# Kernel tuning notes

Hardware: AMD Instinct MI355X
Metric: run time of the kernel (lower is better)

Reference implementation:

```python
import jax, jax.numpy as jnp
import numpy as np

HF = 14            # qubits (hidden_features)
SPECTRUM = 3       # spectrum_layer (data re-uploading blocks)
NSTEPS = 2         # N outer iterations
SEL_L = 3          # StronglyEntanglingLayers depth per block (weights1[..., 3, HF, 3])
DIM = 2 ** HF
BN_EPS = 1e-5

# wire 0 = most-significant bit (PennyLane default.qubit convention)
_bits = ((np.arange(DIM)[:, None] >> (HF - 1 - np.arange(HF))[None, :]) & 1)  # (DIM, HF)
Z_SIGNS = (1.0 - 2.0 * _bits).astype(np.float32)      # +1 for |0>, -1 for |1>
RZ_SIGNS = -Z_SIGNS                                    # (2b-1): RZ phase sign per wire
# CZ ring sign vectors for ranges r=1..SEL_L: (-1)^{sum_j b_j * b_{(j+r)%HF}}
_cz = []
for r in range(1, SEL_L + 1):
    parity = (_bits * _bits[:, (np.arange(HF) + r) % HF]).sum(axis=1) % 2
    _cz.append((1.0 - 2.0 * parity).astype(np.float32))
CZ_SIGNS = np.stack(_cz)  # (SEL_L, DIM)


def _rot_matrix(phi, theta, omega):
    # Rot = RZ(omega) @ RY(theta) @ RZ(phi)
    c = jnp.cos(theta / 2)
    s = jnp.sin(theta / 2)
    ep = jnp.exp(-0.5j * (phi + omega))
    em = jnp.exp(-0.5j * (phi - omega))
    return jnp.array([[ep * c, -jnp.conj(em) * s],
                      [em * s, jnp.conj(ep) * c]])


def _apply_1q(state, U, wire):
    # state: (b, 2^HF) complex; apply 2x2 U on `wire`
    b = state.shape[0]
    st = state.reshape(b, 2 ** wire, 2, -1)
    st = jnp.einsum('pq,bwqm->bwpm', U, st)
    return st.reshape(b, DIM)


def _run_circuit(x, w):
    # x: (b, HF) real RZ angles; w: (SPECTRUM, SEL_L, HF, 3)
    b = x.shape[0]
    state = jnp.zeros((b, DIM), jnp.complex64).at[:, 0].set(1.0)
    rz_diag = jnp.exp(0.5j * (x @ jnp.asarray(RZ_SIGNS).T))  # (b, DIM) complex64
    cz = jnp.asarray(CZ_SIGNS)
    for i in range(SPECTRUM):
        state = state * rz_diag                 # RZ(x_j) on every wire (diagonal)
        for l in range(SEL_L):
            for q in range(HF):
                state = _apply_1q(state, _rot_matrix(w[i, l, q, 0], w[i, l, q, 1], w[i, l, q, 2]), q)
            state = state * cz[l][None, :]      # CZ ring, range l+1 (diagonal +-1)
    probs = jnp.abs(state) ** 2
    return probs @ jnp.asarray(Z_SIGNS)          # <Z_j> per wire, (b, HF)


def setup_inputs() -> dict:
    key = jax.random.key(0)
    ks = jax.random.split(key, 6)
    b, c, w, h = 64, 1, 28, 28
    input_dim = c * w * h
    x = jax.random.normal(ks[0], (b, c, w, h), dtype=jnp.float32)
    w_down = jax.random.normal(ks[1], (HF, input_dim), dtype=jnp.float32) * (1.0 / np.sqrt(input_dim))
    b_down = jax.random.normal(ks[2], (HF,), dtype=jnp.float32) * 0.01
    bn_w = jnp.ones((HF,), jnp.float32)
    bn_b = jnp.zeros((HF,), jnp.float32)
    weights1 = jax.random.normal(ks[3], (NSTEPS, SPECTRUM, SEL_L, HF, 3), dtype=jnp.float32) * 0.4
    w_up = jax.random.normal(ks[4], (input_dim, HF), dtype=jnp.float32) * (1.0 / np.sqrt(HF))
    b_up = jax.random.normal(ks[5], (input_dim,), dtype=jnp.float32) * 0.01
    return {"x": x, "w_down": w_down, "b_down": b_down, "bn_w": bn_w, "bn_b": bn_b,
            "weights1": weights1, "w_up": w_up, "b_up": b_up}


def reference(x, w_down, b_down, bn_w, bn_b, weights1, w_up, b_up):
    b, c, w, h = x.shape
    xr = x.reshape(b, -1) @ w_down.T + b_down          # linear_down -> (b, HF)
    for n in range(NSTEPS):
        mu = xr.mean(axis=0)
        var = ((xr - mu) ** 2).mean(axis=0)            # BatchNorm1d, training-mode batch stats
        xr = (xr - mu) / jnp.sqrt(var + BN_EPS) * bn_w + bn_b
        xr = _run_circuit(xr, weights1[n])             # quantum circuit expvals -> (b, HF)
    out = xr @ w_up.T + b_up                           # linear_up
    return out.reshape(b, c, w, h)
```

## Files before the change

kernel.cpp:

```cpp
#include <hip/hip_runtime.h>
#include <math.h>

#define INV2PI 0.15915494309189535f

typedef _Float16 f16;
typedef _Float16 f16x8 __attribute__((ext_vector_type(8)));
typedef _Float16 f16x4 __attribute__((ext_vector_type(4)));
typedef float f32x16 __attribute__((ext_vector_type(16)));

#define Z16 {0.f,0.f,0.f,0.f,0.f,0.f,0.f,0.f,0.f,0.f,0.f,0.f,0.f,0.f,0.f,0.f}

#define WS_MATS 0
#define WS_TABS 262144
#define WS_RY1  266240
#define WS_XR   266304
#define WS_XR2  267200

__global__ void k_pre(const float* __restrict__ w1, float* __restrict__ ws)
{
    int blk = blockIdx.x, t = threadIdx.x;
    if (blk < 32) {
        int n = blk >> 4, rem = blk & 15, k = (rem >> 1) + 2, side = rem & 1;
        __shared__ float R[7][2][2];
        if (t < 7) {
            int wire = side ? (13 - t) : (6 - t);
            float th = w1[n*378 + (k-1)*42 + wire*3 + 1];
            float s, c; sincosf(0.5f*th, &s, &c);
            R[t][0][0] = c;  R[t][0][1] = -s;
            R[t][1][0] = s;  R[t][1][1] = c;
        }
        __syncthreads();
        f16* M = (f16*)ws + blk * 16384;
        for (int e = t; e < 16384; e += 256) {
            int tile = e >> 12, kk = (e >> 9) & 7, l = (e >> 3) & 63, j = e & 7;
            int row = tile*32 + (l & 31);
            int col = kk*16 + (l >> 5)*8 + j;
            float v = 1.f;
            #pragma unroll
            for (int bi = 0; bi < 7; ++bi) v *= R[bi][(row>>bi)&1][(col>>bi)&1];
            M[e] = (f16)v;
        }
    } else if (blk == 32) {
        for (int e = t; e < 4096; e += 256) {
            int n = e >> 11, r = e & 2047, k = (r >> 8) + 1;
            int r2 = r & 255, side = r2 >> 7, v = r2 & 127;
            float acc = 0.f;
            #pragma unroll
            for (int bi = 0; bi < 7; ++bi) {
                if ((v >> bi) & 1) {
                    int wire = side ? (13 - bi) : (6 - bi);
                    acc += (w1[n*378 + (k-1)*42 + wire*3 + 2]
                          + w1[n*378 + k*42     + wire*3 + 0]) * INV2PI;
                }
            }
            ws[WS_TABS + ((n*8 + (k-1))*2 + side)*128 + v] = acc;
        }
    } else {
        if (t < 28) {
            int n = t / 14, q = t % 14;
            float th = w1[n*378 + q*3 + 1];
            float s, c; sincosf(0.5f*th, &s, &c);
            ws[WS_RY1 + (n*14 + q)*2 + 0] = c;
            ws[WS_RY1 + (n*14 + q)*2 + 1] = s;
        }
    }
}

__global__ void k_down(const float* __restrict__ x, const float* __restrict__ wd,
                       const float* __restrict__ bd, float* __restrict__ xr)
{
    int row  = blockIdx.x;
    int wave = threadIdx.x >> 6;
    int lane = threadIdx.x & 63;
    const float* xrow = x + row * 784;
    for (int f = wave; f < 14; f += 4) {
        const float* wrow = wd + f * 784;
        float s = 0.f;
        for (int j = lane; j < 784; j += 64) s = fmaf(xrow[j], wrow[j], s);
        #pragma unroll
        for (int off = 32; off; off >>= 1) s += __shfl_xor(s, off);
        if (lane == 0) xr[row * 14 + f] = s + bd[f];
    }
}

template<int WHICH>
__global__ __launch_bounds__(1024, 4)
void k_circuit(const f16* __restrict__ matsg, const float* __restrict__ tabsg,
               const float* __restrict__ ry1g, const float* __restrict__ xrin,
               float* __restrict__ xrout, const float* __restrict__ bnw,
               const float* __restrict__ bnb, const float* __restrict__ wu,
               const float* __restrict__ bu)
{
    __shared__ __align__(16) ushort SRe[16384];
    __shared__ __align__(16) ushort SIm[16384];
    __shared__ __align__(16) ushort IRe[16384];
    __shared__ __align__(16) ushort IIm[16384];
    __shared__ float2 ETAB[8][2][128];
    __shared__ float PA[128], PB[128];
    __shared__ float XR[896];
    __shared__ float XROW[14];
    __shared__ float RED[16][15];

    const int row = blockIdx.x, T = threadIdx.x;
    const int w = T >> 6, l = T & 63, lm = l & 31, hb = l >> 5;
    const int tm = w >> 2, tn = w & 3;
    const int mrow = tm*32 + lm, nn = tn*32 + lm;

    for (int i = T; i < 896; i += 1024) XR[i] = xrin[i];
    __syncthreads();
    if (T < 14) {
        float mu = 0.f;
        for (int r = 0; r < 64; ++r) mu += XR[r*14 + T];
        mu *= (1.f/64.f);
        float var = 0.f;
        for (int r = 0; r < 64; ++r) { float d = XR[r*14 + T] - mu; var += d*d; }
        var *= (1.f/64.f);
        float xb = (XR[row*14 + T] - mu) * rsqrtf(var + 1e-5f) * bnw[T] + bnb[T];
        XROW[T] = xb * INV2PI;
    }
    __syncthreads();
    for (int e = T; e < 2048; e += 1024) {
        int k0 = e >> 8, r2 = e & 255, side = r2 >> 7, v = r2 & 127;
        float val = tabsg[(k0*2 + side)*128 + v];
        if (k0 == 2 || k0 == 5) {
            #pragma unroll
            for (int bi = 0; bi < 7; ++bi)
                if ((v >> bi) & 1) val += XROW[side ? (13-bi) : (6-bi)];
        }
        float fr = __builtin_amdgcn_fractf(val);
        ETAB[k0][side][v] = make_float2(__builtin_amdgcn_cosf(fr),
                                        __builtin_amdgcn_sinf(fr));
    }
    if (T < 256) {
        int side = T >> 7, v = T & 127;
        float p = 1.f;
        #pragma unroll
        for (int bi = 0; bi < 7; ++bi) {
            int wire = side ? (13-bi) : (6-bi);
            p *= ((v >> bi) & 1) ? ry1g[wire*2 + 1] : ry1g[wire*2];
        }
        if (side) PB[v] = p; else PA[v] = p;
    }
    __syncthreads();
    {
        int a = T >> 3, b0 = (T & 7) << 4;
        float2 eA = ETAB[0][0][a];
        float pav = PA[a];
        #pragma unroll
        for (int g = 0; g < 2; ++g) {
            f16 hr[8], hm[8];
            #pragma unroll
            for (int u = 0; u < 8; ++u) {
                int b = b0 + g*8 + u;
                int d = (a << 7) | b;
                int rot = ((d >> 1) | (d << 13)) & 16383;
                float2 eB = ETAB[0][1][b];
                float zr = eA.x*eB.x - eA.y*eB.y;
                float zi = eA.x*eB.y + eA.y*eB.x;
                if (__popc(d & rot) & 1) { zr = -zr; zi = -zi; }
                float mg = pav * PB[b];
                hr[u] = (f16)(mg * zr);
                hm[u] = (f16)(mg * zi);
            }
            int hoff = ((a << 7) + b0 + g*8) ^ ((a & 15) << 3);
            f16x8 vr = {hr[0],hr[1],hr[2],hr[3],hr[4],hr[5],hr[6],hr[7]};
            f16x8 vi = {hm[0],hm[1],hm[2],hm[3],hm[4],hm[5],hm[6],hm[7]};
            *(f16x8*)((f16*)SRe + hoff) = vr;
            *(f16x8*)((f16*)SIm + hoff) = vi;
        }
    }
    __syncthreads();

    #pragma unroll 1
    for (int k = 2; k <= 9; ++k) {
        const int P = k & 1;
        const f16* M1 = matsg + ((k-2)*2 + (P ? 0 : 1)) * 16384;
        const f16* M2 = matsg + ((k-2)*2 + (P ? 1 : 0)) * 16384;
        f32x16 ar = Z16, ai = Z16;
        #pragma unroll
        for (int kk = 0; kk < 8; ++kk) {
            f16x8 B = *(const f16x8*)(M1 + (tn*8 + kk)*512 + l*8);
            int c  = kk*16 + hb*8;
            int sa = ((mrow << 7) + c) ^ ((mrow & 15) << 3);
            f16x8 Ar = *(const f16x8*)((const f16*)SRe + sa);
            f16x8 Ai = *(const f16x8*)((const f16*)SIm + sa);
            ar = __builtin_amdgcn_mfma_f32_32x32x16_f16(Ar, B, ar, 0,0,0);
            ai = __builtin_amdgcn_mfma_f32_32x32x16_f16(Ai, B, ai, 0,0,0);
        }
        #pragma unroll
        for (int g = 0; g < 4; ++g) {
            int mb = tm*32 + g*8 + hb*4;
            int hoff = ((nn << 7) + mb) ^ ((nn & 15) << 3);
            f16x4 vr = {(f16)ar[g*4],(f16)ar[g*4+1],(f16)ar[g*4+2],(f16)ar[g*4+3]};
            f16x4 vi = {(f16)ai[g*4],(f16)ai[g*4+1],(f16)ai[g*4+2],(f16)ai[g*4+3]};
            *(f16x4*)((f16*)IRe + hoff) = vr;
            *(f16x4*)((f16*)IIm + hoff) = vi;
        }
        __syncthreads();
        f32x16 dr = Z16, di = Z16;
        #pragma unroll
        for (int kk = 0; kk < 8; ++kk) {
            f16x8 A = *(const f16x8*)(M2 + (tm*8 + kk)*512 + l*8);
            int c  = kk*16 + hb*8;
            int s0 = ((nn << 7) + c) ^ ((nn & 15) << 3);
            f16x8 Br = *(const f16x8*)((const f16*)IRe + s0);
            f16x8 Bi = *(const f16x8*)((const f16*)IIm + s0);
            dr = __builtin_amdgcn_mfma_f32_32x32x16_f16(A, Br, dr, 0,0,0);
            di = __builtin_amdgcn_mfma_f32_32x32x16_f16(A, Bi, di, 0,0,0);
        }
        if (k < 9) {
            float2 eN = ETAB[k-1][P ? 0 : 1][nn];
            const int czr = ((k-1) % 3) + 1;
            #pragma unroll
            for (int g = 0; g < 4; ++g) {
                float prf[4], pif[4];
                #pragma unroll
                for (int u = 0; u < 4; ++u) {
                    int r = g*4 + u;
                    int mloc = (r & 3) + 8*(r >> 2) + 4*hb;
                    int mg = tm*32 + mloc;
                    float2 eM = ETAB[k-1][P ? 1 : 0][mg];
                    int d = P ? ((nn << 7) | mg) : ((mg << 7) | nn);
                    int rot = ((d >> czr) | (d << (14 - czr))) & 16383;
                    float zr = eM.x*eN.x - eM.y*eN.y;
                    float zi = eM.x*eN.y + eM.y*eN.x;
                    if (__popc(d & rot) & 1) { zr = -zr; zi = -zi; }
                    float re = dr[r], im = di[r];
                    prf[u] = re*zr - im*zi;
                    pif[u] = re*zi + im*zr;
                }
                int mb = tm*32 + g*8 + hb*4;
                int hoff = ((nn << 7) + mb) ^ ((nn & 15) << 3);
                f16x4 vr = {(f16)prf[0],(f16)prf[1],(f16)prf[2],(f16)prf[3]};
                f16x4 vi = {(f16)pif[0],(f16)pif[1],(f16)pif[2],(f16)pif[3]};
                *(f16x4*)((f16*)SRe + hoff) = vr;
                *(f16x4*)((f16*)SIm + hoff) = vi;
            }
        } else {
            float tot = 0.f;
            float bs[14];
            #pragma unroll
            for (int i = 0; i < 14; ++i) bs[i] = 0.f;
            float tp = 0.f, s0 = 0.f, s1v = 0.f, s3 = 0.f, s4 = 0.f;
            #pragma unroll
            for (int r = 0; r < 16; ++r) {
                float re = dr[r], im = di[r];
                float p = fmaf(re, re, im*im);
                tp += p;
                if (r & 1) s0  += p;
                if (r & 2) s1v += p;
                if (r & 4) s3  += p;
                if (r & 8) s4  += p;
            }
            tot += tp;
            bs[0] += s0; bs[1] += s1v; bs[3] += s3; bs[4] += s4;
            if (hb)     bs[2] += tp;
            if (tm & 1) bs[5] += tp;
            if (tm & 2) bs[6] += tp;
            #pragma unroll
            for (int i = 0; i < 7; ++i)
                if ((nn >> i) & 1) bs[7+i] += tp;
            #pragma unroll
            for (int off = 32; off; off >>= 1) {
                tot += __shfl_xor(tot, off);
                #pragma unroll
                for (int i = 0; i < 14; ++i) bs[i] += __shfl_xor(bs[i], off);
            }
            if (l == 0) {
                #pragma unroll
                for (int i = 0; i < 14; ++i) RED[w][i] = bs[i];
                RED[w][14] = tot;
            }
        }
        __syncthreads();
    }

    if (T < 14) {
        float tt = 0.f, ss = 0.f;
        #pragma unroll
        for (int ww = 0; ww < 16; ++ww) { tt += RED[ww][14]; ss += RED[ww][13 - T]; }
        float val = tt - 2.f * ss;
        XROW[T] = val;
        if (WHICH == 0) xrout[row*14 + T] = val;
    }
    __syncthreads();
    if (WHICH == 1) {
        for (int j = T; j < 784; j += 1024) {
            float s = bu[j];
            #pragma unroll
            for (int f = 0; f < 14; ++f) s = fmaf(XROW[f], wu[j*14 + f], s);
            xrout[row*784 + j] = s;
        }
    }
}

extern "C" void kernel_launch(void* const* d_in, const int* in_sizes, int n_in,
                              void* d_out, int out_size, void* d_ws, size_t ws_size,
                              hipStream_t stream)
{
    const float* x  = (const float*)d_in[0];
    const float* wd = (const float*)d_in[1];
    const float* bd = (const float*)d_in[2];
    const float* bw = (const float*)d_in[3];
    const float* bb = (const float*)d_in[4];
    const float* w1 = (const float*)d_in[5];
    const float* wu = (const float*)d_in[6];
    const float* bu = (const float*)d_in[7];
    float* out = (float*)d_out;
    float* ws  = (float*)d_ws;

    hipLaunchKernelGGL(k_pre,  dim3(34), dim3(256), 0, stream, w1, ws);
    hipLaunchKernelGGL(k_down, dim3(64), dim3(256), 0, stream, x, wd, bd, ws + WS_XR);

    const f16* mats0 = (const f16*)ws;
    const f16* mats1 = (const f16*)ws + 262144;
    hipLaunchKernelGGL(k_circuit<0>, dim3(64), dim3(1024), 0, stream,
                       mats0, ws + WS_TABS, ws + WS_RY1,
                       ws + WS_XR, ws + WS_XR2, bw, bb, wu, bu);
    hipLaunchKernelGGL(k_circuit<1>, dim3(64), dim3(1024), 0, stream,
                       mats1, ws + WS_TABS + 2048, ws + WS_RY1 + 28,
                       ws + WS_XR2, out, bw, bb, wu, bu);
}
```

Before: 124.3 us.

## Halve circuit block size and give each wave a 32x64 MFMA tile

The circuit kernel drops from 1024 to 512 threads per block. Each wave now computes two 32x32 output tiles, so one LDS A-fragment load feeds two MFMA pairs, which cuts LDS read traffic per MFMA. s_setprio is raised around the MFMA loops to favour the matrix issue. The trade-offs are fewer waves to hide latency, higher register pressure from four accumulators, and more serial work per thread in the setup phases.

```diff
diff --git a/kernel.cpp b/kernel.cpp
--- a/kernel.cpp
+++ b/kernel.cpp
@@ -84,7 +84,7 @@
 }
 
 template<int WHICH>
-__global__ __launch_bounds__(1024, 4)
+__global__ __launch_bounds__(512, 2)
 void k_circuit(const f16* __restrict__ matsg, const float* __restrict__ tabsg,
                const float* __restrict__ ry1g, const float* __restrict__ xrin,
                float* __restrict__ xrout, const float* __restrict__ bnw,
@@ -99,14 +99,14 @@
     __shared__ float PA[128], PB[128];
     __shared__ float XR[896];
     __shared__ float XROW[14];
-    __shared__ float RED[16][15];
+    __shared__ float RED[8][15];
 
     const int row = blockIdx.x, T = threadIdx.x;
     const int w = T >> 6, l = T & 63, lm = l & 31, hb = l >> 5;
-    const int tm = w >> 2, tn = w & 3;
-    const int mrow = tm*32 + lm, nn = tn*32 + lm;
-
-    for (int i = T; i < 896; i += 1024) XR[i] = xrin[i];
+    const int th = w >> 1, tp = w & 1;
+    const int hrow = th*32 + lm;
+
+    for (int i = T; i < 896; i += 512) XR[i] = xrin[i];
     __syncthreads();
     if (T < 14) {
         float mu = 0.f;
@@ -119,7 +119,7 @@
         XROW[T] = xb * INV2PI;
     }
     __syncthreads();
-    for (int e = T; e < 2048; e += 1024) {
+    for (int e = T; e < 2048; e += 512) {
         int k0 = e >> 8, r2 = e & 255, side = r2 >> 7, v = r2 & 127;
         float val = tabsg[(k0*2 + side)*128 + v];
         if (k0 == 2 || k0 == 5) {
@@ -143,11 +143,11 @@
     }
     __syncthreads();
     {
-        int a = T >> 3, b0 = (T & 7) << 4;
+        int a = T >> 2, b0 = (T & 3) << 5;
         float2 eA = ETAB[0][0][a];
         float pav = PA[a];
         #pragma unroll
-        for (int g = 0; g < 2; ++g) {
+        for (int g = 0; g < 4; ++g) {
             f16 hr[8], hm[8];
             #pragma unroll
             for (int u = 0; u < 8; ++u) {
@@ -176,90 +176,117 @@
         const int P = k & 1;
         const f16* M1 = matsg + ((k-2)*2 + (P ? 0 : 1)) * 16384;
         const f16* M2 = matsg + ((k-2)*2 + (P ? 1 : 0)) * 16384;
-        f32x16 ar = Z16, ai = Z16;
+        f32x16 ar0 = Z16, ai0 = Z16, ar1 = Z16, ai1 = Z16;
+        __builtin_amdgcn_s_setprio(1);
         #pragma unroll
         for (int kk = 0; kk < 8; ++kk) {
-            f16x8 B = *(const f16x8*)(M1 + (tn*8 + kk)*512 + l*8);
+            f16x8 B0 = *(const f16x8*)(M1 + ((tp*2+0)<<12) + kk*512 + l*8);
+            f16x8 B1 = *(const f16x8*)(M1 + ((tp*2+1)<<12) + kk*512 + l*8);
             int c  = kk*16 + hb*8;
-            int sa = ((mrow << 7) + c) ^ ((mrow & 15) << 3);
+            int sa = ((hrow << 7) + c) ^ ((hrow & 15) << 3);
             f16x8 Ar = *(const f16x8*)((const f16*)SRe + sa);
             f16x8 Ai = *(const f16x8*)((const f16*)SIm + sa);
-            ar = __builtin_amdgcn_mfma_f32_32x32x16_f16(Ar, B, ar, 0,0,0);
-            ai = __builtin_amdgcn_mfma_f32_32x32x16_f16(Ai, B, ai, 0,0,0);
-        }
-        #pragma unroll
-        for (int g = 0; g < 4; ++g) {
-            int mb = tm*32 + g*8 + hb*4;
-            int hoff = ((nn << 7) + mb) ^ ((nn & 15) << 3);
-            f16x4 vr = {(f16)ar[g*4],(f16)ar[g*4+1],(f16)ar[g*4+2],(f16)ar[g*4+3]};
-            f16x4 vi = {(f16)ai[g*4],(f16)ai[g*4+1],(f16)ai[g*4+2],(f16)ai[g*4+3]};
-            *(f16x4*)((f16*)IRe + hoff) = vr;
-            *(f16x4*)((f16*)IIm + hoff) = vi;
+            ar0 = __builtin_amdgcn_mfma_f32_32x32x16_f16(Ar, B0, ar0, 0,0,0);
+            ai0 = __builtin_amdgcn_mfma_f32_32x32x16_f16(Ai, B0, ai0, 0,0,0);
+            ar1 = __builtin_amdgcn_mfma_f32_32x32x16_f16(Ar, B1, ar1, 0,0,0);
+            ai1 = __builtin_amdgcn_mfma_f32_32x32x16_f16(Ai, B1, ai1, 0,0,0);
+        }
+        __builtin_amdgcn_s_setprio(0);
+        #pragma unroll
+        for (int j = 0; j < 2; ++j) {
+            int nj = (tp*2 + j)*32 + lm;
+            const f32x16& vr = j ? ar1 : ar0;
+            const f32x16& vi = j ? ai1 : ai0;
+            #pragma unroll
+            for (int g = 0; g < 4; ++g) {
+                int mb = th*32 + g*8 + hb*4;
+                int hoff = ((nj << 7) + mb) ^ ((nj & 15) << 3);
+                f16x4 hr = {(f16)vr[g*4],(f16)vr[g*4+1],(f16)vr[g*4+2],(f16)vr[g*4+3]};
+                f16x4 hi = {(f16)vi[g*4],(f16)vi[g*4+1],(f16)vi[g*4+2],(f16)vi[g*4+3]};
+                *(f16x4*)((f16*)IRe + hoff) = hr;
+                *(f16x4*)((f16*)IIm + hoff) = hi;
+            }
         }
         __syncthreads();
-        f32x16 dr = Z16, di = Z16;
+        f32x16 dr0 = Z16, di0 = Z16, dr1 = Z16, di1 = Z16;
+        __builtin_amdgcn_s_setprio(1);
         #pragma unroll
         for (int kk = 0; kk < 8; ++kk) {
-            f16x8 A = *(const f16x8*)(M2 + (tm*8 + kk)*512 + l*8);
+            f16x8 A0 = *(const f16x8*)(M2 + ((tp*2+0)<<12) + kk*512 + l*8);
+            f16x8 A1 = *(const f16x8*)(M2 + ((tp*2+1)<<12) + kk*512 + l*8);
             int c  = kk*16 + hb*8;
-            int s0 = ((nn << 7) + c) ^ ((nn & 15) << 3);
+            int s0 = ((hrow << 7) + c) ^ ((hrow & 15) << 3);
             f16x8 Br = *(const f16x8*)((const f16*)IRe + s0);
             f16x8 Bi = *(const f16x8*)((const f16*)IIm + s0);
-            dr = __builtin_amdgcn_mfma_f32_32x32x16_f16(A, Br, dr, 0,0,0);
-            di = __builtin_amdgcn_mfma_f32_32x32x16_f16(A, Bi, di, 0,0,0);
-        }
+            dr0 = __builtin_amdgcn_mfma_f32_32x32x16_f16(A0, Br, dr0, 0,0,0);
+            di0 = __builtin_amdgcn_mfma_f32_32x32x16_f16(A0, Bi, di0, 0,0,0);
+            dr1 = __builtin_amdgcn_mfma_f32_32x32x16_f16(A1, Br, dr1, 0,0,0);
+            di1 = __builtin_amdgcn_mfma_f32_32x32x16_f16(A1, Bi, di1, 0,0,0);
+        }
+        __builtin_amdgcn_s_setprio(0);
+        const int nn = hrow;
         if (k < 9) {
             float2 eN = ETAB[k-1][P ? 0 : 1][nn];
             const int czr = ((k-1) % 3) + 1;
             #pragma unroll
-            for (int g = 0; g < 4; ++g) {
-                float prf[4], pif[4];
-                #pragma unroll
-                for (int u = 0; u < 4; ++u) {
-                    int r = g*4 + u;
-                    int mloc = (r & 3) + 8*(r >> 2) + 4*hb;
-                    int mg = tm*32 + mloc;
-                    float2 eM = ETAB[k-1][P ? 1 : 0][mg];
-                    int d = P ? ((nn << 7) | mg) : ((mg << 7) | nn);
-                    int rot = ((d >> czr) | (d << (14 - czr))) & 16383;
-                    float zr = eM.x*eN.x - eM.y*eN.y;
-                    float zi = eM.x*eN.y + eM.y*eN.x;
-                    if (__popc(d & rot) & 1) { zr = -zr; zi = -zi; }
-                    float re = dr[r], im = di[r];
-                    prf[u] = re*zr - im*zi;
-                    pif[u] = re*zi + im*zr;
+            for (int j = 0; j < 2; ++j) {
+                const f32x16& dr = j ? dr1 : dr0;
+                const f32x16& di = j ? di1 : di0;
+                #pragma unroll
+                for (int g = 0; g < 4; ++g) {
+                    float prf[4], pif[4];
+                    #pragma unroll
+                    for (int u = 0; u < 4; ++u) {
+                        int r = g*4 + u;
+                        int mloc = (r & 3) + 8*(r >> 2) + 4*hb;
+                        int mg = (tp*2 + j)*32 + mloc;
+                        float2 eM = ETAB[k-1][P ? 1 : 0][mg];
+                        int d = P ? ((nn << 7) | mg) : ((mg << 7) | nn);
+                        int rot = ((d >> czr) | (d << (14 - czr))) & 16383;
+                        float zr = eM.x*eN.x - eM.y*eN.y;
+                        float zi = eM.x*eN.y + eM.y*eN.x;
+                        if (__popc(d & rot) & 1) { zr = -zr; zi = -zi; }
+                        float re = dr[r], im = di[r];
+                        prf[u] = re*zr - im*zi;
+                        pif[u] = re*zi + im*zr;
+                    }
+                    int mb = (tp*2 + j)*32 + g*8 + hb*4;
+                    int hoff = ((nn << 7) + mb) ^ ((nn & 15) << 3);
+                    f16x4 hr = {(f16)prf[0],(f16)prf[1],(f16)prf[2],(f16)prf[3]};
+                    f16x4 hi = {(f16)pif[0],(f16)pif[1],(f16)pif[2],(f16)pif[3]};
+                    *(f16x4*)((f16*)SRe + hoff) = hr;
+                    *(f16x4*)((f16*)SIm + hoff) = hi;
                 }
-                int mb = tm*32 + g*8 + hb*4;
-                int hoff = ((nn << 7) + mb) ^ ((nn & 15) << 3);
-                f16x4 vr = {(f16)prf[0],(f16)prf[1],(f16)prf[2],(f16)prf[3]};
-                f16x4 vi = {(f16)pif[0],(f16)pif[1],(f16)pif[2],(f16)pif[3]};
-                *(f16x4*)((f16*)SRe + hoff) = vr;
-                *(f16x4*)((f16*)SIm + hoff) = vi;
             }
         } else {
             float tot = 0.f;
             float bs[14];
             #pragma unroll
             for (int i = 0; i < 14; ++i) bs[i] = 0.f;
-            float tp = 0.f, s0 = 0.f, s1v = 0.f, s3 = 0.f, s4 = 0.f;
-            #pragma unroll
-            for (int r = 0; r < 16; ++r) {
-                float re = dr[r], im = di[r];
-                float p = fmaf(re, re, im*im);
-                tp += p;
-                if (r & 1) s0  += p;
-                if (r & 2) s1v += p;
-                if (r & 4) s3  += p;
-                if (r & 8) s4  += p;
-            }
-            tot += tp;
-            bs[0] += s0; bs[1] += s1v; bs[3] += s3; bs[4] += s4;
-            if (hb)     bs[2] += tp;
-            if (tm & 1) bs[5] += tp;
-            if (tm & 2) bs[6] += tp;
-            #pragma unroll
-            for (int i = 0; i < 7; ++i)
-                if ((nn >> i) & 1) bs[7+i] += tp;
+            #pragma unroll
+            for (int j = 0; j < 2; ++j) {
+                const f32x16& dr = j ? dr1 : dr0;
+                const f32x16& di = j ? di1 : di0;
+                float tp2 = 0.f, s0 = 0.f, s1v = 0.f, s3 = 0.f, s4 = 0.f;
+                #pragma unroll
+                for (int r = 0; r < 16; ++r) {
+                    float re = dr[r], im = di[r];
+                    float p = fmaf(re, re, im*im);
+                    tp2 += p;
+                    if (r & 1) s0  += p;
+                    if (r & 2) s1v += p;
+                    if (r & 4) s3  += p;
+                    if (r & 8) s4  += p;
+                }
+                tot += tp2;
+                bs[0] += s0; bs[1] += s1v; bs[3] += s3; bs[4] += s4;
+                if (hb) bs[2] += tp2;
+                if (j)  bs[5] += tp2;
+                if (tp) bs[6] += tp2;
+                #pragma unroll
+                for (int i = 0; i < 7; ++i)
+                    if ((nn >> i) & 1) bs[7+i] += tp2;
+            }
             #pragma unroll
             for (int off = 32; off; off >>= 1) {
                 tot += __shfl_xor(tot, off);
@@ -278,14 +305,14 @@
     if (T < 14) {
         float tt = 0.f, ss = 0.f;
         #pragma unroll
-        for (int ww = 0; ww < 16; ++ww) { tt += RED[ww][14]; ss += RED[ww][13 - T]; }
+        for (int ww = 0; ww < 8; ++ww) { tt += RED[ww][14]; ss += RED[ww][13 - T]; }
         float val = tt - 2.f * ss;
         XROW[T] = val;
         if (WHICH == 0) xrout[row*14 + T] = val;
     }
     __syncthreads();
     if (WHICH == 1) {
-        for (int j = T; j < 784; j += 1024) {
+        for (int j = T; j < 784; j += 512) {
             float s = bu[j];
             #pragma unroll
             for (int f = 0; f < 14; ++f) s = fmaf(XROW[f], wu[j*14 + f], s);
@@ -314,10 +341,10 @@
 
     const f16* mats0 = (const f16*)ws;
     const f16* mats1 = (const f16*)ws + 262144;
-    hipLaunchKernelGGL(k_circuit<0>, dim3(64), dim3(1024), 0, stream,
+    hipLaunchKernelGGL(k_circuit<0>, dim3(64), dim3(512), 0, stream,
                        mats0, ws + WS_TABS, ws + WS_RY1,
                        ws + WS_XR, ws + WS_XR2, bw, bb, wu, bu);
-    hipLaunchKernelGGL(k_circuit<1>, dim3(64), dim3(1024), 0, stream,
+    hipLaunchKernelGGL(k_circuit<1>, dim3(64), dim3(512), 0, stream,
                        mats1, ws + WS_TABS + 2048, ws + WS_RY1 + 28,
                        ws + WS_XR2, out, bw, bb, wu, bu);
 }
```

After: 139.4 us. 1.12x slower.

## Fold weight-only phase into complex second-stage matrix and rebalance first GEMM

Applied to the files above, without the earlier changes.

The precompute kernel now folds the weight-dependent diagonal phase and part of the CZ sign into a complex second-side rotation matrix (separate real and imaginary halves), so the per-element epilogue only handles the input-dependent phase and a cheap bitmask sign. The first GEMM is re-split so half the waves handle the real part and half the imaginary part, each computing two N tiles with shared A loads. The second GEMM becomes a complex-by-complex product with four MFMAs per step, doubling its matrix work and global matrix reads in exchange for a much lighter epilogue. Workspace layout and offsets grow to hold the extra matrices.

```diff
diff --git a/kernel.cpp b/kernel.cpp
--- a/kernel.cpp
+++ b/kernel.cpp
@@ -10,37 +10,73 @@
 
 #define Z16 {0.f,0.f,0.f,0.f,0.f,0.f,0.f,0.f,0.f,0.f,0.f,0.f,0.f,0.f,0.f,0.f}
 
-#define WS_MATS 0
-#define WS_TABS 262144
-#define WS_RY1  266240
-#define WS_XR   266304
-#define WS_XR2  267200
+#define WS_MATS  0
+#define WS_TABS  393216
+#define WS_RY1   397312
+#define WS_XR    397440
+#define WS_XR2   398400
 
 __global__ void k_pre(const float* __restrict__ w1, float* __restrict__ ws)
 {
     int blk = blockIdx.x, t = threadIdx.x;
-    if (blk < 32) {
-        int n = blk >> 4, rem = blk & 15, k = (rem >> 1) + 2, side = rem & 1;
-        __shared__ float R[7][2][2];
-        if (t < 7) {
-            int wire = side ? (13 - t) : (6 - t);
+    if (blk < 16) {
+        int n = blk >> 3, k = (blk & 7) + 2, P = k & 1;
+        int side1 = P ? 0 : 1;
+        int side2 = P ? 1 : 0;
+        __shared__ float RS[2][7][2][2];
+        __shared__ float2 ZM[128];
+        if (t < 14) {
+            int role = t / 7, bi = t % 7;
+            int side = role ? side2 : side1;
+            int wire = side ? (13 - bi) : (6 - bi);
             float th = w1[n*378 + (k-1)*42 + wire*3 + 1];
             float s, c; sincosf(0.5f*th, &s, &c);
-            R[t][0][0] = c;  R[t][0][1] = -s;
-            R[t][1][0] = s;  R[t][1][1] = c;
+            RS[role][bi][0][0] = c;  RS[role][bi][0][1] = -s;
+            RS[role][bi][1][0] = s;  RS[role][bi][1][1] = c;
+        }
+        if (t >= 64 && t < 192 && k < 9) {
+            int v = t - 64;
+            float alpha = 0.f;
+            #pragma unroll
+            for (int bi = 0; bi < 7; ++bi) {
+                if ((v >> bi) & 1) {
+                    int wire = side2 ? (13 - bi) : (6 - bi);
+                    alpha += (w1[n*378 + (k-1)*42 + wire*3 + 2]
+                            + w1[n*378 + k*42     + wire*3 + 0]) * INV2PI;
+                }
+            }
+            int rc = ((k - 1) % 3) + 1;
+            int sg = __popc(v & (v >> rc) & ((1 << (7 - rc)) - 1)) & 1;
+            float fr = __builtin_amdgcn_fractf(alpha);
+            float c = __builtin_amdgcn_cosf(fr);
+            float s = __builtin_amdgcn_sinf(fr);
+            ZM[v] = sg ? make_float2(-c, -s) : make_float2(c, s);
         }
         __syncthreads();
-        f16* M = (f16*)ws + blk * 16384;
+        f16* p0 = (f16*)ws + (n*8 + (k-2)) * 49152;
+        f16* p1 = p0 + 16384;
+        f16* p2 = p1 + 16384;
         for (int e = t; e < 16384; e += 256) {
             int tile = e >> 12, kk = (e >> 9) & 7, l = (e >> 3) & 63, j = e & 7;
             int row = tile*32 + (l & 31);
             int col = kk*16 + (l >> 5)*8 + j;
-            float v = 1.f;
-            #pragma unroll
-            for (int bi = 0; bi < 7; ++bi) v *= R[bi][(row>>bi)&1][(col>>bi)&1];
-            M[e] = (f16)v;
-        }
-    } else if (blk == 32) {
+            float v1 = 1.f, v2 = 1.f;
+            #pragma unroll
+            for (int bi = 0; bi < 7; ++bi) {
+                int rb = (row >> bi) & 1, cb = (col >> bi) & 1;
+                v1 *= RS[0][bi][rb][cb];
+                v2 *= RS[1][bi][rb][cb];
+            }
+            p0[e] = (f16)v1;
+            if (k < 9) {
+                float2 z = ZM[row];
+                p1[e] = (f16)(v2 * z.x);
+                p2[e] = (f16)(v2 * z.y);
+            } else {
+                p1[e] = (f16)v2;
+            }
+        }
+    } else {
         for (int e = t; e < 4096; e += 256) {
             int n = e >> 11, r = e & 2047, k = (r >> 8) + 1;
             int r2 = r & 255, side = r2 >> 7, v = r2 & 127;
@@ -55,7 +91,6 @@
             }
             ws[WS_TABS + ((n*8 + (k-1))*2 + side)*128 + v] = acc;
         }
-    } else {
         if (t < 28) {
             int n = t / 14, q = t % 14;
             float th = w1[n*378 + q*3 + 1];
@@ -96,6 +131,7 @@
     __shared__ __align__(16) ushort IRe[16384];
     __shared__ __align__(16) ushort IIm[16384];
     __shared__ float2 ETAB[8][2][128];
+    __shared__ float2 EXM[2][128];
     __shared__ float PA[128], PB[128];
     __shared__ float XR[896];
     __shared__ float XROW[14];
@@ -105,6 +141,9 @@
     const int w = T >> 6, l = T & 63, lm = l & 31, hb = l >> 5;
     const int tm = w >> 2, tn = w & 3;
     const int mrow = tm*32 + lm, nn = tn*32 + lm;
+    const int comp = w >> 3, w3 = w & 7;
+    const int tmS = w3 >> 1, tpS = w3 & 1;
+    const int hrowS = tmS*32 + lm;
 
     for (int i = T; i < 896; i += 1024) XR[i] = xrin[i];
     __syncthreads();
@@ -128,8 +167,13 @@
                 if ((v >> bi) & 1) val += XROW[side ? (13-bi) : (6-bi)];
         }
         float fr = __builtin_amdgcn_fractf(val);
-        ETAB[k0][side][v] = make_float2(__builtin_amdgcn_cosf(fr),
-                                        __builtin_amdgcn_sinf(fr));
+        float c = __builtin_amdgcn_cosf(fr);
+        float s = __builtin_amdgcn_sinf(fr);
+        if (k0 >= 1 && side == (k0 & 1)) {
+            int rc = (k0 % 3) + 1;
+            if (__popc(v & (v >> rc) & ((1 << (7 - rc)) - 1)) & 1) { c = -c; s = -s; }
+        }
+        ETAB[k0][side][v] = make_float2(c, s);
     }
     if (T < 256) {
         int side = T >> 7, v = T & 127;
@@ -140,6 +184,15 @@
             p *= ((v >> bi) & 1) ? ry1g[wire*2 + 1] : ry1g[wire*2];
         }
         if (side) PB[v] = p; else PA[v] = p;
+    } else if (T < 512) {
+        int e = T - 256, side = e >> 7, v = e & 127;
+        float xs = 0.f;
+        #pragma unroll
+        for (int bi = 0; bi < 7; ++bi)
+            if ((v >> bi) & 1) xs += XROW[side ? (13-bi) : (6-bi)];
+        float fr = __builtin_amdgcn_fractf(xs);
+        EXM[side][v] = make_float2(__builtin_amdgcn_cosf(fr),
+                                   __builtin_amdgcn_sinf(fr));
     }
     __syncthreads();
     {
@@ -174,60 +227,85 @@
     #pragma unroll 1
     for (int k = 2; k <= 9; ++k) {
         const int P = k & 1;
-        const f16* M1 = matsg + ((k-2)*2 + (P ? 0 : 1)) * 16384;
-        const f16* M2 = matsg + ((k-2)*2 + (P ? 1 : 0)) * 16384;
-        f32x16 ar = Z16, ai = Z16;
-        #pragma unroll
-        for (int kk = 0; kk < 8; ++kk) {
-            f16x8 B = *(const f16x8*)(M1 + (tn*8 + kk)*512 + l*8);
-            int c  = kk*16 + hb*8;
-            int sa = ((mrow << 7) + c) ^ ((mrow & 15) << 3);
-            f16x8 Ar = *(const f16x8*)((const f16*)SRe + sa);
-            f16x8 Ai = *(const f16x8*)((const f16*)SIm + sa);
-            ar = __builtin_amdgcn_mfma_f32_32x32x16_f16(Ar, B, ar, 0,0,0);
-            ai = __builtin_amdgcn_mfma_f32_32x32x16_f16(Ai, B, ai, 0,0,0);
-        }
-        #pragma unroll
-        for (int g = 0; g < 4; ++g) {
-            int mb = tm*32 + g*8 + hb*4;
-            int hoff = ((nn << 7) + mb) ^ ((nn & 15) << 3);
-            f16x4 vr = {(f16)ar[g*4],(f16)ar[g*4+1],(f16)ar[g*4+2],(f16)ar[g*4+3]};
-            f16x4 vi = {(f16)ai[g*4],(f16)ai[g*4+1],(f16)ai[g*4+2],(f16)ai[g*4+3]};
-            *(f16x4*)((f16*)IRe + hoff) = vr;
-            *(f16x4*)((f16*)IIm + hoff) = vi;
+        const f16* M1  = matsg + (k-2)*49152;
+        const f16* M2r = M1 + 16384;
+        const f16* M2i = M2r + 16384;
+        {
+            const ushort* Sp = comp ? SIm : SRe;
+            ushort* Ip = comp ? IIm : IRe;
+            f32x16 a0 = Z16, a1 = Z16;
+            #pragma unroll
+            for (int kk = 0; kk < 8; ++kk) {
+                int c  = kk*16 + hb*8;
+                int sa = ((hrowS << 7) + c) ^ ((hrowS & 15) << 3);
+                f16x8 A  = *(const f16x8*)((const f16*)Sp + sa);
+                f16x8 B0 = *(const f16x8*)(M1 + ((tpS*2+0)*8 + kk)*512 + l*8);
+                f16x8 B1 = *(const f16x8*)(M1 + ((tpS*2+1)*8 + kk)*512 + l*8);
+                a0 = __builtin_amdgcn_mfma_f32_32x32x16_f16(A, B0, a0, 0,0,0);
+                a1 = __builtin_amdgcn_mfma_f32_32x32x16_f16(A, B1, a1, 0,0,0);
+            }
+            #pragma unroll
+            for (int j = 0; j < 2; ++j) {
+                int nj = (tpS*2 + j)*32 + lm;
+                const f32x16& va = j ? a1 : a0;
+                #pragma unroll
+                for (int g = 0; g < 4; ++g) {
+                    int mb = tmS*32 + g*8 + hb*4;
+                    int hoff = ((nj << 7) + mb) ^ ((nj & 15) << 3);
+                    f16x4 hv = {(f16)va[g*4],(f16)va[g*4+1],(f16)va[g*4+2],(f16)va[g*4+3]};
+                    *(f16x4*)((f16*)Ip + hoff) = hv;
+                }
+            }
         }
         __syncthreads();
-        f32x16 dr = Z16, di = Z16;
-        #pragma unroll
-        for (int kk = 0; kk < 8; ++kk) {
-            f16x8 A = *(const f16x8*)(M2 + (tm*8 + kk)*512 + l*8);
-            int c  = kk*16 + hb*8;
-            int s0 = ((nn << 7) + c) ^ ((nn & 15) << 3);
-            f16x8 Br = *(const f16x8*)((const f16*)IRe + s0);
-            f16x8 Bi = *(const f16x8*)((const f16*)IIm + s0);
-            dr = __builtin_amdgcn_mfma_f32_32x32x16_f16(A, Br, dr, 0,0,0);
-            di = __builtin_amdgcn_mfma_f32_32x32x16_f16(A, Bi, di, 0,0,0);
-        }
         if (k < 9) {
-            float2 eN = ETAB[k-1][P ? 0 : 1][nn];
-            const int czr = ((k-1) % 3) + 1;
+            f32x16 dr = Z16, di = Z16;
+            #pragma unroll
+            for (int kk = 0; kk < 8; ++kk) {
+                int c  = kk*16 + hb*8;
+                int s0 = ((nn << 7) + c) ^ ((nn & 15) << 3);
+                f16x8 Br = *(const f16x8*)((const f16*)IRe + s0);
+                f16x8 Bi = *(const f16x8*)((const f16*)IIm + s0);
+                f16x8 Ar = *(const f16x8*)(M2r + (tm*8 + kk)*512 + l*8);
+                f16x8 Ai = *(const f16x8*)(M2i + (tm*8 + kk)*512 + l*8);
+                f16x8 AiN = -Ai;
+                dr = __builtin_amdgcn_mfma_f32_32x32x16_f16(Ar,  Br, dr, 0,0,0);
+                dr = __builtin_amdgcn_mfma_f32_32x32x16_f16(AiN, Bi, dr, 0,0,0);
+                di = __builtin_amdgcn_mfma_f32_32x32x16_f16(Ar,  Bi, di, 0,0,0);
+                di = __builtin_amdgcn_mfma_f32_32x32x16_f16(Ai,  Br, di, 0,0,0);
+            }
+            const int k0 = k - 1;
+            const int czr = (k0 % 3) + 1;
+            const bool xl = (k == 3) || (k == 6);
+            const int msd = k & 1;
+            float2 zN = ETAB[k0][k0 & 1][nn];
+            int mrc = (1 << czr) - 1;
+            int CM = ((nn >> (7 - czr)) & mrc) | ((nn & mrc) << (7 - czr));
+            int w16 = 0;
+            if (CM & 1)  w16 ^= 0xAAAA;
+            if (CM & 2)  w16 ^= 0xCCCC;
+            if (CM & 8)  w16 ^= 0xF0F0;
+            if (CM & 16) w16 ^= 0xFF00;
+            if (__popc(((tm << 5) | (hb << 2)) & CM) & 1) w16 ^= 0xFFFF;
             #pragma unroll
             for (int g = 0; g < 4; ++g) {
                 float prf[4], pif[4];
                 #pragma unroll
                 for (int u = 0; u < 4; ++u) {
                     int r = g*4 + u;
-                    int mloc = (r & 3) + 8*(r >> 2) + 4*hb;
-                    int mg = tm*32 + mloc;
-                    float2 eM = ETAB[k-1][P ? 1 : 0][mg];
-                    int d = P ? ((nn << 7) | mg) : ((mg << 7) | nn);
-                    int rot = ((d >> czr) | (d << (14 - czr))) & 16383;
-                    float zr = eM.x*eN.x - eM.y*eN.y;
-                    float zi = eM.x*eN.y + eM.y*eN.x;
-                    if (__popc(d & rot) & 1) { zr = -zr; zi = -zi; }
+                    float zr = zN.x, zi = zN.y;
+                    if (xl) {
+                        int mg = tm*32 + (r & 3) + 8*(r >> 2) + 4*hb;
+                        float2 em = EXM[msd][mg];
+                        float t0 = em.x*zN.x - em.y*zN.y;
+                        float t1 = em.x*zN.y + em.y*zN.x;
+                        zr = t0; zi = t1;
+                    }
                     float re = dr[r], im = di[r];
-                    prf[u] = re*zr - im*zi;
-                    pif[u] = re*zi + im*zr;
+                    float pr = re*zr - im*zi;
+                    float pi = re*zi + im*zr;
+                    if ((w16 >> r) & 1) { pr = -pr; pi = -pi; }
+                    prf[u] = pr; pif[u] = pi;
                 }
                 int mb = tm*32 + g*8 + hb*4;
                 int hoff = ((nn << 7) + mb) ^ ((nn & 15) << 3);
@@ -237,23 +315,34 @@
                 *(f16x4*)((f16*)SIm + hoff) = vi;
             }
         } else {
+            f32x16 dr = Z16, di = Z16;
+            #pragma unroll
+            for (int kk = 0; kk < 8; ++kk) {
+                int c  = kk*16 + hb*8;
+                int s0 = ((nn << 7) + c) ^ ((nn & 15) << 3);
+                f16x8 Br = *(const f16x8*)((const f16*)IRe + s0);
+                f16x8 Bi = *(const f16x8*)((const f16*)IIm + s0);
+                f16x8 A  = *(const f16x8*)(M2r + (tm*8 + kk)*512 + l*8);
+                dr = __builtin_amdgcn_mfma_f32_32x32x16_f16(A, Br, dr, 0,0,0);
+                di = __builtin_amdgcn_mfma_f32_32x32x16_f16(A, Bi, di, 0,0,0);
+            }
             float tot = 0.f;
             float bs[14];
             #pragma unroll
             for (int i = 0; i < 14; ++i) bs[i] = 0.f;
-            float tp = 0.f, s0 = 0.f, s1v = 0.f, s3 = 0.f, s4 = 0.f;
+            float tp = 0.f, s0v = 0.f, s1v = 0.f, s3 = 0.f, s4 = 0.f;
             #pragma unroll
             for (int r = 0; r < 16; ++r) {
                 float re = dr[r], im = di[r];
                 float p = fmaf(re, re, im*im);
                 tp += p;
-                if (r & 1) s0  += p;
+                if (r & 1) s0v += p;
                 if (r & 2) s1v += p;
                 if (r & 4) s3  += p;
                 if (r & 8) s4  += p;
             }
             tot += tp;
-            bs[0] += s0; bs[1] += s1v; bs[3] += s3; bs[4] += s4;
+            bs[0] += s0v; bs[1] += s1v; bs[3] += s3; bs[4] += s4;
             if (hb)     bs[2] += tp;
             if (tm & 1) bs[5] += tp;
             if (tm & 2) bs[6] += tp;
@@ -309,11 +398,11 @@
     float* out = (float*)d_out;
     float* ws  = (float*)d_ws;
 
-    hipLaunchKernelGGL(k_pre,  dim3(34), dim3(256), 0, stream, w1, ws);
+    hipLaunchKernelGGL(k_pre,  dim3(17), dim3(256), 0, stream, w1, ws);
     hipLaunchKernelGGL(k_down, dim3(64), dim3(256), 0, stream, x, wd, bd, ws + WS_XR);
 
     const f16* mats0 = (const f16*)ws;
-    const f16* mats1 = (const f16*)ws + 262144;
+    const f16* mats1 = (const f16*)ws + 393216;
     hipLaunchKernelGGL(k_circuit<0>, dim3(64), dim3(1024), 0, stream,
                        mats0, ws + WS_TABS, ws + WS_RY1,
                        ws + WS_XR, ws + WS_XR2, bw, bb, wu, bu);
```

After: 150.3 us. +20.9%, slower.

## Fold CZ sign factors into matrices and phase tables; split first GEMM by component

Applied to the files above, without the earlier changes.

The CZ ring's ±1 sign is split into three parts. The part that depends only on the high or low 7-bit half is folded into the precomputed rotation matrices and the ETAB phase table. The cross-half part becomes a per-lane 16-bit mask, so the inner loop no longer computes a popcount per element. The first MFMA stage is also reorganised so each wave handles one component (real or imaginary) and two N-tiles, sharing the A fragment across two MFMAs instead of sharing B across re/im. This trims per-element ALU work in the epilogue and changes LDS/global load patterns. The price is more complex sign bookkeeping, which is a correctness risk.

```diff
diff --git a/kernel.cpp b/kernel.cpp
--- a/kernel.cpp
+++ b/kernel.cpp
@@ -21,6 +21,9 @@
     int blk = blockIdx.x, t = threadIdx.x;
     if (blk < 32) {
         int n = blk >> 4, rem = blk & 15, k = (rem >> 1) + 2, side = rem & 1;
+        int side2 = (k & 1) ? 1 : 0;
+        bool fold = (side == side2) && (k < 9);
+        int rc = ((k - 1) % 3) + 1;
         __shared__ float R[7][2][2];
         if (t < 7) {
             int wire = side ? (13 - t) : (6 - t);
@@ -38,6 +41,8 @@
             float v = 1.f;
             #pragma unroll
             for (int bi = 0; bi < 7; ++bi) v *= R[bi][(row>>bi)&1][(col>>bi)&1];
+            if (fold && (__popc(row & (row >> rc) & ((1 << (7 - rc)) - 1)) & 1))
+                v = -v;
             M[e] = (f16)v;
         }
     } else if (blk == 32) {
@@ -104,7 +109,10 @@
     const int row = blockIdx.x, T = threadIdx.x;
     const int w = T >> 6, l = T & 63, lm = l & 31, hb = l >> 5;
     const int tm = w >> 2, tn = w & 3;
-    const int mrow = tm*32 + lm, nn = tn*32 + lm;
+    const int nn = tn*32 + lm;
+    const int comp = w >> 3, w3 = w & 7;
+    const int tmS = w3 >> 1, tpS = w3 & 1;
+    const int hrowS = tmS*32 + lm;
 
     for (int i = T; i < 896; i += 1024) XR[i] = xrin[i];
     __syncthreads();
@@ -128,8 +136,13 @@
                 if ((v >> bi) & 1) val += XROW[side ? (13-bi) : (6-bi)];
         }
         float fr = __builtin_amdgcn_fractf(val);
-        ETAB[k0][side][v] = make_float2(__builtin_amdgcn_cosf(fr),
-                                        __builtin_amdgcn_sinf(fr));
+        float c = __builtin_amdgcn_cosf(fr);
+        float s = __builtin_amdgcn_sinf(fr);
+        if (k0 >= 1 && side == (k0 & 1)) {
+            int rc = (k0 % 3) + 1;
+            if (__popc(v & (v >> rc) & ((1 << (7 - rc)) - 1)) & 1) { c = -c; s = -s; }
+        }
+        ETAB[k0][side][v] = make_float2(c, s);
     }
     if (T < 256) {
         int side = T >> 7, v = T & 127;
@@ -176,25 +189,32 @@
         const int P = k & 1;
         const f16* M1 = matsg + ((k-2)*2 + (P ? 0 : 1)) * 16384;
         const f16* M2 = matsg + ((k-2)*2 + (P ? 1 : 0)) * 16384;
-        f32x16 ar = Z16, ai = Z16;
-        #pragma unroll
-        for (int kk = 0; kk < 8; ++kk) {
-            f16x8 B = *(const f16x8*)(M1 + (tn*8 + kk)*512 + l*8);
-            int c  = kk*16 + hb*8;
-            int sa = ((mrow << 7) + c) ^ ((mrow & 15) << 3);
-            f16x8 Ar = *(const f16x8*)((const f16*)SRe + sa);
-            f16x8 Ai = *(const f16x8*)((const f16*)SIm + sa);
-            ar = __builtin_amdgcn_mfma_f32_32x32x16_f16(Ar, B, ar, 0,0,0);
-            ai = __builtin_amdgcn_mfma_f32_32x32x16_f16(Ai, B, ai, 0,0,0);
-        }
-        #pragma unroll
-        for (int g = 0; g < 4; ++g) {
-            int mb = tm*32 + g*8 + hb*4;
-            int hoff = ((nn << 7) + mb) ^ ((nn & 15) << 3);
-            f16x4 vr = {(f16)ar[g*4],(f16)ar[g*4+1],(f16)ar[g*4+2],(f16)ar[g*4+3]};
-            f16x4 vi = {(f16)ai[g*4],(f16)ai[g*4+1],(f16)ai[g*4+2],(f16)ai[g*4+3]};
-            *(f16x4*)((f16*)IRe + hoff) = vr;
-            *(f16x4*)((f16*)IIm + hoff) = vi;
+        {
+            const ushort* Sp = comp ? SIm : SRe;
+            ushort* Ip = comp ? IIm : IRe;
+            f32x16 a0 = Z16, a1 = Z16;
+            #pragma unroll
+            for (int kk = 0; kk < 8; ++kk) {
+                int c  = kk*16 + hb*8;
+                int sa = ((hrowS << 7) + c) ^ ((hrowS & 15) << 3);
+                f16x8 A  = *(const f16x8*)((const f16*)Sp + sa);
+                f16x8 B0 = *(const f16x8*)(M1 + ((tpS*2+0)*8 + kk)*512 + l*8);
+                f16x8 B1 = *(const f16x8*)(M1 + ((tpS*2+1)*8 + kk)*512 + l*8);
+                a0 = __builtin_amdgcn_mfma_f32_32x32x16_f16(A, B0, a0, 0,0,0);
+                a1 = __builtin_amdgcn_mfma_f32_32x32x16_f16(A, B1, a1, 0,0,0);
+            }
+            #pragma unroll
+            for (int j = 0; j < 2; ++j) {
+                int nj = (tpS*2 + j)*32 + lm;
+                const f32x16& va = j ? a1 : a0;
+                #pragma unroll
+                for (int g = 0; g < 4; ++g) {
+                    int mb = tmS*32 + g*8 + hb*4;
+                    int hoff = ((nj << 7) + mb) ^ ((nj & 15) << 3);
+                    f16x4 hv = {(f16)va[g*4],(f16)va[g*4+1],(f16)va[g*4+2],(f16)va[g*4+3]};
+                    *(f16x4*)((f16*)Ip + hoff) = hv;
+                }
+            }
         }
         __syncthreads();
         f32x16 dr = Z16, di = Z16;
@@ -209,8 +229,18 @@
             di = __builtin_amdgcn_mfma_f32_32x32x16_f16(A, Bi, di, 0,0,0);
         }
         if (k < 9) {
-            float2 eN = ETAB[k-1][P ? 0 : 1][nn];
-            const int czr = ((k-1) % 3) + 1;
+            const int k0 = k - 1;
+            const int czr = (k0 % 3) + 1;
+            float2 eN = ETAB[k0][P ? 0 : 1][nn];
+            const float* eMt = (const float*)&ETAB[k0][P ? 1 : 0][0];
+            int mrc = (1 << czr) - 1;
+            int CM = ((nn >> (7 - czr)) & mrc) | ((nn & mrc) << (7 - czr));
+            int w16 = 0;
+            if (CM & 1)  w16 ^= 0xAAAA;
+            if (CM & 2)  w16 ^= 0xCCCC;
+            if (CM & 8)  w16 ^= 0xF0F0;
+            if (CM & 16) w16 ^= 0xFF00;
+            if (__popc(((tm << 5) | (hb << 2)) & CM) & 1) w16 ^= 0xFFFF;
             #pragma unroll
             for (int g = 0; g < 4; ++g) {
                 float prf[4], pif[4];
@@ -219,15 +249,14 @@
                     int r = g*4 + u;
                     int mloc = (r & 3) + 8*(r >> 2) + 4*hb;
                     int mg = tm*32 + mloc;
-                    float2 eM = ETAB[k-1][P ? 1 : 0][mg];
-                    int d = P ? ((nn << 7) | mg) : ((mg << 7) | nn);
-                    int rot = ((d >> czr) | (d << (14 - czr))) & 16383;
+                    float2 eM = *(const float2*)(eMt + 2*mg);
                     float zr = eM.x*eN.x - eM.y*eN.y;
                     float zi = eM.x*eN.y + eM.y*eN.x;
-                    if (__popc(d & rot) & 1) { zr = -zr; zi = -zi; }
                     float re = dr[r], im = di[r];
-                    prf[u] = re*zr - im*zi;
-                    pif[u] = re*zi + im*zr;
+                    float pr = re*zr - im*zi;
+                    float pi = re*zi + im*zr;
+                    if ((w16 >> r) & 1) { pr = -pr; pi = -pi; }
+                    prf[u] = pr; pif[u] = pi;
                 }
                 int mb = tm*32 + g*8 + hb*4;
                 int hoff = ((nn << 7) + mb) ^ ((nn & 15) << 3);
@@ -241,19 +270,19 @@
             float bs[14];
             #pragma unroll
             for (int i = 0; i < 14; ++i) bs[i] = 0.f;
-            float tp = 0.f, s0 = 0.f, s1v = 0.f, s3 = 0.f, s4 = 0.f;
+            float tp = 0.f, s0v = 0.f, s1v = 0.f, s3 = 0.f, s4 = 0.f;
             #pragma unroll
             for (int r = 0; r < 16; ++r) {
                 float re = dr[r], im = di[r];
                 float p = fmaf(re, re, im*im);
                 tp += p;
-                if (r & 1) s0  += p;
+                if (r & 1) s0v += p;
                 if (r & 2) s1v += p;
                 if (r & 4) s3  += p;
                 if (r & 8) s4  += p;
             }
             tot += tp;
-            bs[0] += s0; bs[1] += s1v; bs[3] += s3; bs[4] += s4;
+            bs[0] += s0v; bs[1] += s1v; bs[3] += s3; bs[4] += s4;
             if (hb)     bs[2] += tp;
             if (tm & 1) bs[5] += tp;
             if (tm & 2) bs[6] += tp;
```

New measurement: 126.8 us. Within noise of the previous version (+2.0%).
